# Kernel optimization log

Hardware: AMD Instinct MI355X
Metric: run time of the kernel (lower is better)

The kernel has to match this reference:

```python
import jax, jax.numpy as jnp
import numpy as np

N, C_IN, D, K, C_OUT = 50000, 256, 25000, 16, 256


def setup_inputs() -> dict:
    key = jax.random.key(0)
    k1, k2, k3, k4 = jax.random.split(key, 4)
    x = jax.random.normal(k1, (N, C_IN), dtype=jnp.float32)
    symm_norm = jax.random.uniform(k2, (N,), dtype=jnp.float32)
    domains = jax.random.randint(k3, (D, K), 0, N, dtype=jnp.int64)
    # Linear params: in = 2*C_IN (order-1 transfer doubles channels), xavier-uniform
    fan_in, fan_out = 2 * C_IN, C_OUT
    limit = float(np.sqrt(6.0 / (fan_in + fan_out)))
    w = jax.random.uniform(k4, (2 * C_IN, C_OUT), dtype=jnp.float32,
                           minval=-limit, maxval=limit)
    b = jnp.zeros((C_OUT,), dtype=jnp.float32)
    return {"x": x, "symm_norm": symm_norm, "domains": domains, "w": w, "b": b}


def reference(x, symm_norm, domains, w, b):
    # symmetric normalization: outer(features, symm_norm) -> per-node scale
    xs = x * symm_norm[:, None]                      # [N, C]
    # transfer1 (ptensors1 over singleton domains -> ptensors1 over target domains):
    # gather node features into each target domain; the two order-1 linmaps
    # (identity, broadcast-of-sum over the singleton intersection) coincide.
    g = jnp.take(xs, domains, axis=0)                # [D, K, C]
    f = jnp.concatenate([g, g], axis=-1)             # [D, K, 2C]
    # linear projection
    y = jnp.einsum('dkc,co->dko', f, w) + b          # [D, K, C_OUT]
    return y
```

## Files before the change

kernel.cpp:

```cpp
#include <hip/hip_runtime.h>


#define GM 50000
#define GK 256
#define GN 256
#define BM 128
#define BN 128
#define BK 16
#define LDA (BM + 4)
#define LDB (BN + 4)

__global__ __launch_bounds__(256, 4)
void gemm_z_kernel(const float* __restrict__ x,
                   const float* __restrict__ sn,
                   const float* __restrict__ w,
                   const float* __restrict__ b,
                   float* __restrict__ z) {
    __shared__ float As[BK][LDA];
    __shared__ float Bs[BK][LDB];

    const int t  = threadIdx.x;
    const int tx = t & 15;
    const int ty = t >> 4;
    const int rowBase = blockIdx.x * BM;
    const int colBase = blockIdx.y * BN;

    const int a_m = t >> 2;
    const int a_k = (t & 3) * 4;
    const int b_k = t >> 5;
    const int b_n = (t & 31) * 4;

    float acc[8][8] = {};

    for (int k0 = 0; k0 < GK; k0 += BK) {
        #pragma unroll
        for (int h = 0; h < 2; ++h) {
            const int mr = a_m + h * 64;
            const int m  = rowBase + mr;
            float4 v = make_float4(0.f, 0.f, 0.f, 0.f);
            if (m < GM) {
                v = *reinterpret_cast<const float4*>(&x[(size_t)m * GK + k0 + a_k]);
                const float s = sn[m];
                v.x *= s; v.y *= s; v.z *= s; v.w *= s;
            }
            As[a_k + 0][mr] = v.x;
            As[a_k + 1][mr] = v.y;
            As[a_k + 2][mr] = v.z;
            As[a_k + 3][mr] = v.w;
        }
        #pragma unroll
        for (int h = 0; h < 2; ++h) {
            const int kk = b_k + h * 8;
            const int gk = k0 + kk;
            const int gn = colBase + b_n;
            float4 v0 = *reinterpret_cast<const float4*>(&w[(size_t)gk * GN + gn]);
            float4 v1 = *reinterpret_cast<const float4*>(&w[(size_t)(gk + 256) * GN + gn]);
            v0.x += v1.x; v0.y += v1.y; v0.z += v1.z; v0.w += v1.w;
            *reinterpret_cast<float4*>(&Bs[kk][b_n]) = v0;
        }
        __syncthreads();

        #pragma unroll
        for (int kk = 0; kk < BK; ++kk) {
            float a[8], bb[8];
            *reinterpret_cast<float4*>(&a[0])  =
                *reinterpret_cast<const float4*>(&As[kk][ty * 4]);
            *reinterpret_cast<float4*>(&a[4])  =
                *reinterpret_cast<const float4*>(&As[kk][64 + ty * 4]);
            *reinterpret_cast<float4*>(&bb[0]) =
                *reinterpret_cast<const float4*>(&Bs[kk][tx * 4]);
            *reinterpret_cast<float4*>(&bb[4]) =
                *reinterpret_cast<const float4*>(&Bs[kk][64 + tx * 4]);
            #pragma unroll
            for (int i = 0; i < 8; ++i)
                #pragma unroll
                for (int j = 0; j < 8; ++j)
                    acc[i][j] += a[i] * bb[j];
        }
        __syncthreads();
    }

    const int n0 = colBase + tx * 4;
    const float4 bias0 = *reinterpret_cast<const float4*>(&b[n0]);
    const float4 bias1 = *reinterpret_cast<const float4*>(&b[n0 + 64]);
    #pragma unroll
    for (int i = 0; i < 8; ++i) {
        const int m = rowBase + (i >> 2) * 64 + ty * 4 + (i & 3);
        if (m >= GM) continue;
        float* zr = &z[(size_t)m * GN];
        float4 v;
        v.x = acc[i][0] + bias0.x; v.y = acc[i][1] + bias0.y;
        v.z = acc[i][2] + bias0.z; v.w = acc[i][3] + bias0.w;
        *reinterpret_cast<float4*>(&zr[n0]) = v;
        v.x = acc[i][4] + bias1.x; v.y = acc[i][5] + bias1.y;
        v.z = acc[i][6] + bias1.z; v.w = acc[i][7] + bias1.w;
        *reinterpret_cast<float4*>(&zr[n0 + 64]) = v;
    }
}

__global__ __launch_bounds__(256)
void gather_kernel(const float* __restrict__ z,
                   const int* __restrict__ domains,
                   float* __restrict__ out,
                   int R) {
    const int r = blockIdx.x * 4 + (threadIdx.x >> 6);
    if (r >= R) return;
    const int c = (threadIdx.x & 63) * 4;
    const int n = domains[r];
    const float4 v = *reinterpret_cast<const float4*>(&z[(size_t)n * GN + c]);
    *reinterpret_cast<float4*>(&out[(size_t)r * GN + c]) = v;
}

extern "C" void kernel_launch(void* const* d_in, const int* in_sizes, int n_in,
                              void* d_out, int out_size, void* d_ws, size_t ws_size,
                              hipStream_t stream) {
    const float* x  = (const float*)d_in[0];
    const float* sn = (const float*)d_in[1];
    const int*   dm = (const int*)d_in[2];
    const float* w  = (const float*)d_in[3];
    const float* b  = (const float*)d_in[4];
    float* out = (float*)d_out;
    float* z   = (float*)d_ws;

    dim3 gemm_grid((GM + BM - 1) / BM, GN / BN);
    gemm_z_kernel<<<gemm_grid, 256, 0, stream>>>(x, sn, w, b, z);

    const int R = 25000 * 16;
    gather_kernel<<<(R + 3) / 4, 256, 0, stream>>>(z, dm, out, R);
}
```

Measured before the change: 586.7 us.

## Scatter GEMM results directly to output rows via inverted domain index

Builds an inverted index from node to the output rows that reference it, using atomic counters and fixed-capacity buckets. The GEMM epilogue then writes each projected node row straight to all of its output positions with nontemporal stores. This removes the intermediate z write and the separate gather pass that re-read z. Nodes with more than the bucket capacity fall back to z plus a small cleanup kernel. The cost is two extra small kernels with atomics, and epilogue scatter loops whose trip counts differ across lanes within a wave.

```diff
diff --git a/kernel.cpp b/kernel.cpp
--- a/kernel.cpp
+++ b/kernel.cpp
@@ -4,18 +4,49 @@
 #define GM 50000
 #define GK 256
 #define GN 256
+#define RTOT 400000
 #define BM 128
 #define BN 128
 #define BK 16
 #define LDA (BM + 4)
 #define LDB (BN + 4)
+#define CAP 64
+#define OVF_MAX 4096
+
+typedef float v4f __attribute__((ext_vector_type(4)));
+
+__global__ __launch_bounds__(256)
+void zero_kernel(int* __restrict__ cnt, int* __restrict__ ovf_cnt) {
+    const int i = blockIdx.x * 256 + threadIdx.x;
+    if (i < GM) cnt[i] = 0;
+    if (i == 0) *ovf_cnt = 0;
+}
+
+__global__ __launch_bounds__(256)
+void build_kernel(const int* __restrict__ dm, int* __restrict__ cnt,
+                  int* __restrict__ bucket, int* __restrict__ ovf,
+                  int* __restrict__ ovf_cnt) {
+    const int r = blockIdx.x * 256 + threadIdx.x;
+    if (r >= RTOT) return;
+    const int n = dm[r];
+    const int slot = atomicAdd(&cnt[n], 1);
+    if (slot < CAP) {
+        bucket[n * CAP + slot] = r;
+    } else {
+        const int o = atomicAdd(ovf_cnt, 1);
+        if (o < OVF_MAX) ovf[o] = r;
+    }
+}
 
 __global__ __launch_bounds__(256, 4)
-void gemm_z_kernel(const float* __restrict__ x,
-                   const float* __restrict__ sn,
-                   const float* __restrict__ w,
-                   const float* __restrict__ b,
-                   float* __restrict__ z) {
+void gemm_scatter_kernel(const float* __restrict__ x,
+                         const float* __restrict__ sn,
+                         const float* __restrict__ w,
+                         const float* __restrict__ b,
+                         const int* __restrict__ cnt,
+                         const int* __restrict__ bucket,
+                         float* __restrict__ out,
+                         float* __restrict__ z) {
     __shared__ float As[BK][LDA];
     __shared__ float Bs[BK][LDB];
 
@@ -87,28 +118,43 @@
     for (int i = 0; i < 8; ++i) {
         const int m = rowBase + (i >> 2) * 64 + ty * 4 + (i & 3);
         if (m >= GM) continue;
-        float* zr = &z[(size_t)m * GN];
-        float4 v;
-        v.x = acc[i][0] + bias0.x; v.y = acc[i][1] + bias0.y;
-        v.z = acc[i][2] + bias0.z; v.w = acc[i][3] + bias0.w;
-        *reinterpret_cast<float4*>(&zr[n0]) = v;
-        v.x = acc[i][4] + bias1.x; v.y = acc[i][5] + bias1.y;
-        v.z = acc[i][6] + bias1.z; v.w = acc[i][7] + bias1.w;
-        *reinterpret_cast<float4*>(&zr[n0 + 64]) = v;
+        v4f v0, v1;
+        v0.x = acc[i][0] + bias0.x; v0.y = acc[i][1] + bias0.y;
+        v0.z = acc[i][2] + bias0.z; v0.w = acc[i][3] + bias0.w;
+        v1.x = acc[i][4] + bias1.x; v1.y = acc[i][5] + bias1.y;
+        v1.z = acc[i][6] + bias1.z; v1.w = acc[i][7] + bias1.w;
+        const int c  = cnt[m];
+        const int cc = c < CAP ? c : CAP;
+        const int* bk = &bucket[m * CAP];
+        for (int j = 0; j < cc; ++j) {
+            const int r = bk[j];
+            float* orow = &out[(size_t)r * GN];
+            __builtin_nontemporal_store(v0, reinterpret_cast<v4f*>(&orow[n0]));
+            __builtin_nontemporal_store(v1, reinterpret_cast<v4f*>(&orow[n0 + 64]));
+        }
+        if (c > CAP) {
+            float* zr = &z[(size_t)m * GN];
+            *reinterpret_cast<v4f*>(&zr[n0])      = v0;
+            *reinterpret_cast<v4f*>(&zr[n0 + 64]) = v1;
+        }
     }
 }
 
 __global__ __launch_bounds__(256)
-void gather_kernel(const float* __restrict__ z,
-                   const int* __restrict__ domains,
-                   float* __restrict__ out,
-                   int R) {
-    const int r = blockIdx.x * 4 + (threadIdx.x >> 6);
-    if (r >= R) return;
-    const int c = (threadIdx.x & 63) * 4;
-    const int n = domains[r];
-    const float4 v = *reinterpret_cast<const float4*>(&z[(size_t)n * GN + c]);
-    *reinterpret_cast<float4*>(&out[(size_t)r * GN + c]) = v;
+void cleanup_kernel(const float* __restrict__ z, const int* __restrict__ dm,
+                    const int* __restrict__ ovf, const int* __restrict__ ovf_cnt,
+                    float* __restrict__ out) {
+    int nov = *ovf_cnt;
+    if (nov > OVF_MAX) nov = OVF_MAX;
+    const int lane = threadIdx.x & 63;
+    const int wid  = (blockIdx.x * 256 + threadIdx.x) >> 6;
+    const int nw   = (gridDim.x * 256) >> 6;
+    for (int i = wid; i < nov; i += nw) {
+        const int r = ovf[i];
+        const int n = dm[r];
+        const float4 v = *reinterpret_cast<const float4*>(&z[(size_t)n * GN + lane * 4]);
+        *reinterpret_cast<float4*>(&out[(size_t)r * GN + lane * 4]) = v;
+    }
 }
 
 extern "C" void kernel_launch(void* const* d_in, const int* in_sizes, int n_in,
@@ -120,11 +166,19 @@
     const float* w  = (const float*)d_in[3];
     const float* b  = (const float*)d_in[4];
     float* out = (float*)d_out;
-    float* z   = (float*)d_ws;
+
+    char* ws = (char*)d_ws;
+    float* z      = (float*)ws;
+    int*   cnt    = (int*)(ws + 51200000);
+    int*   bucket = cnt + GM;
+    int*   ovf_cnt= bucket + (size_t)GM * CAP;
+    int*   ovf    = ovf_cnt + 4;
+
+    zero_kernel<<<(GM + 255) / 256, 256, 0, stream>>>(cnt, ovf_cnt);
+    build_kernel<<<(RTOT + 255) / 256, 256, 0, stream>>>(dm, cnt, bucket, ovf, ovf_cnt);
 
     dim3 gemm_grid((GM + BM - 1) / BM, GN / BN);
-    gemm_z_kernel<<<gemm_grid, 256, 0, stream>>>(x, sn, w, b, z);
+    gemm_scatter_kernel<<<gemm_grid, 256, 0, stream>>>(x, sn, w, b, cnt, bucket, out, z);
 
-    const int R = 25000 * 16;
-    gather_kernel<<<(R + 3) / 4, 256, 0, stream>>>(z, dm, out, R);
+    cleanup_kernel<<<64, 256, 0, stream>>>(z, dm, ovf, ovf_cnt, out);
 }
```

After: 539.7 us. 8.0% less time.
